# Optimization experiments

Measured on AMD Instinct MI355X. Metric: run time of the kernel, lower is better.

Reference implementation:

```python
import jax, jax.numpy as jnp
import numpy as np

B, S, D, H = 8, 2048, 1024, 64  # batch, seq, dimension, attention_head_size


def setup_inputs() -> dict:
    key = jax.random.key(0)
    k0, k1, k2, k3 = jax.random.split(key, 4)
    scale = 1.0 / np.sqrt(D)  # keep activations sane
    return {
        "x": jax.random.normal(k0, (B, S, D), dtype=jnp.float32),
        "Wq": jax.random.normal(k1, (D, H), dtype=jnp.float32) * scale,
        "Wk": jax.random.normal(k2, (D, H), dtype=jnp.float32) * scale,
        "Wv": jax.random.normal(k3, (D, H), dtype=jnp.float32) * scale,
    }


def reference(x, Wq, Wk, Wv):
    # Linear projections (bias=False); W stored as [D, H] == torch weight.T
    q = jnp.einsum("bsd,dh->bsh", x, Wq)
    k = jnp.einsum("bsd,dh->bsh", x, Wk)
    v = jnp.einsum("bsd,dh->bsh", x, Wv)
    # full score matrix, scaled by sqrt(head_size)
    scores = jnp.einsum("bqh,bkh->bqk", q, k) / jnp.sqrt(jnp.float32(H))
    weights = jax.nn.softmax(scores, axis=-1)  # [B, S, S]
    # dropout p=0.0 (eval): identity
    out = jnp.einsum("bqk,bkh->bqh", weights, v)  # [B, S, H]
    return out, weights
```

## Files before the change

kernel.cpp:

```cpp
#include <hip/hip_runtime.h>

#define SB 8
#define SS 2048
#define SD 1024
#define SH 64

typedef float f32x4 __attribute__((ext_vector_type(4)));
typedef __bf16 bf16x8 __attribute__((ext_vector_type(8)));

__device__ __forceinline__ unsigned short f2bf(float f) {
  union { float f; unsigned int u; } v; v.f = f;
  unsigned int u = v.u;
  unsigned int r = u + 0x7FFFu + ((u >> 16) & 1u);
  return (unsigned short)(r >> 16);
}

__global__ void prep_wt(const float* __restrict__ Wq, const float* __restrict__ Wk,
                        const float* __restrict__ Wv, unsigned short* __restrict__ Wt) {
  int idx = blockIdx.x * 256 + threadIdx.x;
  int hc = idx >> 10, d = idx & 1023;
  const float* W = (hc < 64) ? Wq : (hc < 128) ? Wk : Wv;
  int h = hc & 63;
  Wt[idx] = f2bf(W[d * SH + h]);
}

__global__ void __launch_bounds__(512, 2) proj(
    const float* __restrict__ x, const unsigned short* __restrict__ Wt,
    unsigned short* __restrict__ Q, unsigned short* __restrict__ K,
    unsigned short* __restrict__ Vt) {
  __shared__ unsigned short xs[2][32 * 64];
  __shared__ unsigned short Bl[2][192 * 64];

  int tid = threadIdx.x;
  int w = tid >> 6, lane = tid & 63;
  int l15 = lane & 15, kg = lane >> 4;
  int wr = w >> 2, wc = w & 3;
  int m0 = blockIdx.x * 32;

  int srow = tid >> 4, sseg = tid & 15;
  const float* xp = x + (size_t)(m0 + srow) * SD + sseg * 4;
  int swoff = srow * 64 + (((sseg >> 1) ^ (srow & 7)) << 3) + ((sseg & 1) << 2);

#define STAGEB(tt, buf)                                                          \
  {                                                                              \
    _Pragma("unroll") for (int j = 0; j < 3; ++j) {                              \
      int Lb = w * 1024 + j * 8192 + lane * 16;                                  \
      int c = Lb >> 7, cb = Lb & 127;                                            \
      const char* srcp = (const char*)Wt + (size_t)c * 2048 + (tt) * 128 +       \
                         (cb ^ ((c & 7) << 4));                                  \
      __builtin_amdgcn_global_load_lds(                                          \
          (const __attribute__((address_space(1))) unsigned int*)(const void*)srcp, \
          (__attribute__((address_space(3))) unsigned int*)(void*)                \
              ((char*)&Bl[(buf)][0] + w * 1024 + j * 8192),                      \
          16, 0, 0);                                                             \
    }                                                                            \
  }

#define CVTW(RA, buf)                                                           \
  {                                                                             \
    ushort4 cv;                                                                 \
    cv.x = f2bf((RA).x); cv.y = f2bf((RA).y);                                   \
    cv.z = f2bf((RA).z); cv.w = f2bf((RA).w);                                   \
    *(ushort4*)(&xs[(buf)][0] + swoff) = cv;                                    \
  }

  f32x4 acc[3];
#pragma unroll
  for (int nt = 0; nt < 3; ++nt) acc[nt] = f32x4{0.f, 0.f, 0.f, 0.f};

  float4 ra = *(const float4*)xp;
  STAGEB(0, 0);
  CVTW(ra, 0);
  ra = *(const float4*)(xp + 64);
  __syncthreads();

  for (int t = 0; t < 16; ++t) {
    int cur = t & 1, nxt = (t + 1) & 1;
    if (t < 15) CVTW(ra, nxt);
    if (t < 14) ra = *(const float4*)(xp + (t + 2) * 64);
    if (t < 15) STAGEB(t + 1, nxt);

    const char* Bb = (const char*)&Bl[cur][0];
#pragma unroll
    for (int ks = 0; ks < 2; ++ks) {
      int row = wr * 16 + l15;
      int cg = ks * 4 + kg;
      bf16x8 af = *(const bf16x8*)(&xs[cur][0] + row * 64 + ((cg ^ (row & 7)) << 3));
#pragma unroll
      for (int nt = 0; nt < 3; ++nt) {
        int c = wc * 48 + nt * 16 + l15;
        int kb = (ks * 32 + kg * 8) * 2;
        bf16x8 bfr = *(const bf16x8*)(Bb + c * 128 + (kb ^ ((c & 7) << 4)));
        acc[nt] = __builtin_amdgcn_mfma_f32_16x16x32_bf16(af, bfr, acc[nt], 0, 0, 0);
      }
    }
    __syncthreads();
  }

#pragma unroll
  for (int nt = 0; nt < 3; ++nt) {
    int c = wc * 48 + nt * 16 + l15;
    int mat = c >> 6, h = c & 63;
#pragma unroll
    for (int r = 0; r < 4; ++r) {
      int row = m0 + wr * 16 + kg * 4 + r;
      unsigned short bv = f2bf(acc[nt][r]);
      if (mat == 0) {
        Q[(size_t)row * SH + h] = bv;
      } else if (mat == 1) {
        K[(size_t)row * SH + h] = bv;
      } else {
        int bb = row >> 11, key = row & 2047;
        Vt[((size_t)bb * SH + h) * SS + key] = bv;
      }
    }
  }
}

__global__ void __launch_bounds__(512, 4) attn(
    const unsigned short* __restrict__ Q, const unsigned short* __restrict__ Kb,
    const unsigned short* __restrict__ Vt, float* __restrict__ out,
    float* __restrict__ wts) {
  __shared__ __align__(16) float shbuf[8 * 16 * 68];
  __shared__ float mS[8][16], sgS[8][16];
  unsigned short (*psh)[16][72] = (unsigned short (*)[16][72])shbuf;
  float (*cf)[16][68] = (float (*)[16][68])shbuf;

  int b = blockIdx.x & 7, rg = blockIdx.x >> 3;
  int w = threadIdx.x >> 6, lane = threadIdx.x & 63;
  int l15 = lane & 15, kg = lane >> 4;
  int q0 = rg * 16;
  int kv0 = w * 256;

  const unsigned short* Qb  = Q  + (size_t)b * SS * SH;
  const unsigned short* Kbb = Kb + (size_t)b * SS * SH;
  const unsigned short* Vtb = Vt + (size_t)b * SH * SS;

  bf16x8 qf[2];
#pragma unroll
  for (int ks = 0; ks < 2; ++ks)
    qf[ks] = *(const bf16x8*)(Qb + (size_t)(q0 + l15) * SH + ks * 32 + kg * 8);

  f32x4 s[4][4];
#pragma unroll
  for (int kt = 0; kt < 4; ++kt)
#pragma unroll
    for (int n = 0; n < 4; ++n) s[kt][n] = f32x4{0.f, 0.f, 0.f, 0.f};

  for (int kt = 0; kt < 4; ++kt) {
#pragma unroll
    for (int ks = 0; ks < 2; ++ks)
#pragma unroll
      for (int n = 0; n < 4; ++n) {
        bf16x8 kf = *(const bf16x8*)(Kbb + (size_t)(kv0 + kt * 64 + n * 16 + l15) * SH + ks * 32 + kg * 8);
        s[kt][n] = __builtin_amdgcn_mfma_f32_16x16x32_bf16(qf[ks], kf, s[kt][n], 0, 0, 0);
      }
  }

  float m[4], sg[4];
#pragma unroll
  for (int r = 0; r < 4; ++r) {
    float mloc = -1e30f;
#pragma unroll
    for (int kt = 0; kt < 4; ++kt)
#pragma unroll
      for (int n = 0; n < 4; ++n) mloc = fmaxf(mloc, s[kt][n][r]);
    mloc *= 0.125f;
#pragma unroll
    for (int off = 1; off < 16; off <<= 1) mloc = fmaxf(mloc, __shfl_xor(mloc, off));
    float ssum = 0.f;
#pragma unroll
    for (int kt = 0; kt < 4; ++kt)
#pragma unroll
      for (int n = 0; n < 4; ++n) {
        float e = __expf(s[kt][n][r] * 0.125f - mloc);
        s[kt][n][r] = e;
        ssum += e;
      }
#pragma unroll
    for (int off = 1; off < 16; off <<= 1) ssum += __shfl_xor(ssum, off);
    m[r] = mloc; sg[r] = ssum;
  }

  if (l15 == 0) {
#pragma unroll
    for (int r = 0; r < 4; ++r) {
      mS[w][kg * 4 + r] = m[r];
      sgS[w][kg * 4 + r] = sg[r];
    }
  }
  __syncthreads();

  float scal[4];
#pragma unroll
  for (int r = 0; r < 4; ++r) {
    int row = kg * 4 + r;
    float M = -1e30f;
#pragma unroll
    for (int ww = 0; ww < 8; ++ww) M = fmaxf(M, mS[ww][row]);
    float Sg = 0.f;
#pragma unroll
    for (int ww = 0; ww < 8; ++ww) Sg += sgS[ww][row] * __expf(mS[ww][row] - M);
    scal[r] = __expf(m[r] - M) / Sg;
  }

  float* wb = wts + (size_t)b * SS * SS;
  f32x4 oacc[4];
#pragma unroll
  for (int nh = 0; nh < 4; ++nh) oacc[nh] = f32x4{0.f, 0.f, 0.f, 0.f};

  for (int kt = 0; kt < 4; ++kt) {
#pragma unroll
    for (int n = 0; n < 4; ++n)
#pragma unroll
      for (int r = 0; r < 4; ++r) {
        float p = s[kt][n][r] * scal[r];
        wb[(size_t)(q0 + kg * 4 + r) * SS + kv0 + kt * 64 + n * 16 + l15] = p;
        psh[w][kg * 4 + r][n * 16 + l15] = f2bf(p);
      }

#pragma unroll
    for (int ks = 0; ks < 2; ++ks) {
      bf16x8 pu = *(const bf16x8*)&psh[w][l15][ks * 32 + kg * 8];
#pragma unroll
      for (int nh = 0; nh < 4; ++nh) {
        bf16x8 vf = *(const bf16x8*)(Vtb + (size_t)(nh * 16 + l15) * SS + kv0 + kt * 64 + ks * 32 + kg * 8);
        oacc[nh] = __builtin_amdgcn_mfma_f32_16x16x32_bf16(pu, vf, oacc[nh], 0, 0, 0);
      }
    }
  }

  __syncthreads();
#pragma unroll
  for (int nh = 0; nh < 4; ++nh)
#pragma unroll
    for (int r = 0; r < 4; ++r)
      cf[w][kg * 4 + r][nh * 16 + l15] = oacc[nh][r];
  __syncthreads();

  int tid = threadIdx.x;
#pragma unroll
  for (int half = 0; half < 2; ++half) {
    int e = tid + half * 512;
    int row = e >> 6, col = e & 63;
    float ssum = 0.f;
#pragma unroll
    for (int ww = 0; ww < 8; ++ww) ssum += cf[ww][row][col];
    out[((size_t)b * SS + q0 + row) * SH + col] = ssum;
  }
}

extern "C" void kernel_launch(void* const* d_in, const int* in_sizes, int n_in,
                              void* d_out, int out_size, void* d_ws, size_t ws_size,
                              hipStream_t stream) {
  const float* x  = (const float*)d_in[0];
  const float* Wq = (const float*)d_in[1];
  const float* Wk = (const float*)d_in[2];
  const float* Wv = (const float*)d_in[3];

  unsigned short* Wt = (unsigned short*)d_ws;
  unsigned short* Q  = Wt + 192 * 1024;
  unsigned short* K  = Q + 16384 * 64;
  unsigned short* Vt = K + 16384 * 64;

  float* out = (float*)d_out;
  float* wts = out + (size_t)SB * SS * SH;

  prep_wt<<<768, 256, 0, stream>>>(Wq, Wk, Wv, Wt);
  proj<<<512, 512, 0, stream>>>(x, Wt, Q, K, Vt);
  attn<<<1024, 512, 0, stream>>>(Q, K, Vt, out, wts);
}
```

Measured before the change: 96.06 us.

## Stage softmax weights in swizzled LDS for coalesced 16-byte global stores

Each wave now handles interleaved 64-key chunks so that, per kt step, the block jointly covers a contiguous 512-key span. The normalized probabilities go as fp32 into an XOR-swizzled LDS tile. The tile is then written to the weights matrix with 16-byte vector stores that cover full rows, replacing scattered 4-byte stores. The bf16 MFMA operand is rebuilt from the same LDS tile. This adds two block-wide barriers per kt iteration and extra LDS traffic, aiming to make the large weights write more bandwidth-efficient.

```diff
diff --git a/kernel.cpp b/kernel.cpp
--- a/kernel.cpp
+++ b/kernel.cpp
@@ -121,16 +121,14 @@
     const unsigned short* __restrict__ Q, const unsigned short* __restrict__ Kb,
     const unsigned short* __restrict__ Vt, float* __restrict__ out,
     float* __restrict__ wts) {
-  __shared__ __align__(16) float shbuf[8 * 16 * 68];
+  __shared__ __align__(16) float arena[8 * 16 * 68];
   __shared__ float mS[8][16], sgS[8][16];
-  unsigned short (*psh)[16][72] = (unsigned short (*)[16][72])shbuf;
-  float (*cf)[16][68] = (float (*)[16][68])shbuf;
+  float (*cf)[16][68] = (float (*)[16][68])arena;
 
   int b = blockIdx.x & 7, rg = blockIdx.x >> 3;
   int w = threadIdx.x >> 6, lane = threadIdx.x & 63;
   int l15 = lane & 15, kg = lane >> 4;
   int q0 = rg * 16;
-  int kv0 = w * 256;
 
   const unsigned short* Qb  = Q  + (size_t)b * SS * SH;
   const unsigned short* Kbb = Kb + (size_t)b * SS * SH;
@@ -148,11 +146,12 @@
     for (int n = 0; n < 4; ++n) s[kt][n] = f32x4{0.f, 0.f, 0.f, 0.f};
 
   for (int kt = 0; kt < 4; ++kt) {
+    int kbase = kt * 512 + w * 64;
 #pragma unroll
     for (int ks = 0; ks < 2; ++ks)
 #pragma unroll
       for (int n = 0; n < 4; ++n) {
-        bf16x8 kf = *(const bf16x8*)(Kbb + (size_t)(kv0 + kt * 64 + n * 16 + l15) * SH + ks * 32 + kg * 8);
+        bf16x8 kf = *(const bf16x8*)(Kbb + (size_t)(kbase + n * 16 + l15) * SH + ks * 32 + kg * 8);
         s[kt][n] = __builtin_amdgcn_mfma_f32_16x16x32_bf16(qf[ks], kf, s[kt][n], 0, 0, 0);
       }
   }
@@ -210,27 +209,47 @@
   for (int nh = 0; nh < 4; ++nh) oacc[nh] = f32x4{0.f, 0.f, 0.f, 0.f};
 
   for (int kt = 0; kt < 4; ++kt) {
+    int kbase = kt * 512 + w * 64;
+
 #pragma unroll
     for (int n = 0; n < 4; ++n)
 #pragma unroll
       for (int r = 0; r < 4; ++r) {
-        float p = s[kt][n][r] * scal[r];
-        wb[(size_t)(q0 + kg * 4 + r) * SS + kv0 + kt * 64 + n * 16 + l15] = p;
-        psh[w][kg * 4 + r][n * 16 + l15] = f2bf(p);
+        int row = kg * 4 + r;
+        int col = w * 64 + n * 16 + l15;
+        int c4 = col >> 2;
+        arena[row * 512 + (((c4 ^ (row & 7))) << 2) + (col & 3)] = s[kt][n][r] * scal[r];
       }
 
 #pragma unroll
     for (int ks = 0; ks < 2; ++ks) {
-      bf16x8 pu = *(const bf16x8*)&psh[w][l15][ks * 32 + kg * 8];
+      int c4a = (w * 64 + ks * 32 + kg * 8) >> 2;
+      f32x4 pa = *(const f32x4*)&arena[l15 * 512 + ((c4a ^ (l15 & 7)) << 2)];
+      f32x4 pb = *(const f32x4*)&arena[l15 * 512 + (((c4a + 1) ^ (l15 & 7)) << 2)];
+      union { unsigned short us[8]; bf16x8 v; } pu;
+#pragma unroll
+      for (int i = 0; i < 4; ++i) { pu.us[i] = f2bf(pa[i]); pu.us[4 + i] = f2bf(pb[i]); }
 #pragma unroll
       for (int nh = 0; nh < 4; ++nh) {
-        bf16x8 vf = *(const bf16x8*)(Vtb + (size_t)(nh * 16 + l15) * SS + kv0 + kt * 64 + ks * 32 + kg * 8);
-        oacc[nh] = __builtin_amdgcn_mfma_f32_16x16x32_bf16(pu, vf, oacc[nh], 0, 0, 0);
-      }
-    }
-  }
-
-  __syncthreads();
+        bf16x8 vf = *(const bf16x8*)(Vtb + (size_t)(nh * 16 + l15) * SS + kbase + ks * 32 + kg * 8);
+        oacc[nh] = __builtin_amdgcn_mfma_f32_16x16x32_bf16(pu.v, vf, oacc[nh], 0, 0, 0);
+      }
+    }
+
+    __syncthreads();
+
+#pragma unroll
+    for (int i = 0; i < 4; ++i) {
+      int flat = w * 4 + i;
+      int row = flat >> 1, half = flat & 1;
+      int c4 = half * 64 + lane;
+      f32x4 v4 = *(const f32x4*)&arena[row * 512 + ((c4 ^ (row & 7)) << 2)];
+      *(f32x4*)(wb + (size_t)(q0 + row) * SS + kt * 512 + half * 256 + lane * 4) = v4;
+    }
+
+    __syncthreads();
+  }
+
 #pragma unroll
   for (int nh = 0; nh < 4; ++nh)
 #pragma unroll
```

Result: no change. 96.83 us (+0.8%).
